# Optimization experiments

Measured on AMD Instinct MI355X. Metric: run time of the kernel, lower is better.

## Reference

```python
import jax, jax.numpy as jnp
import numpy as np

B, S, D = 1, 2048, 2048
H = 16
HD = D // H           # 128
FFN_H = 5632          # int(2*4*D/3) rounded up to multiple of 256
EPS = 1e-5
ROPE_THETA = 10000.0


def rms_norm(x, w, eps=EPS):
    # x * rsqrt(mean(x^2, -1) + eps) * w
    return x * jax.lax.rsqrt(jnp.mean(x * x, axis=-1, keepdims=True) + eps) * w


def apply_rope(x, cos, sin):
    # x: [B, S, H, HD]; cos/sin: [S, HD//2]
    b, s, h, hd = x.shape
    xr = x.reshape(b, s, h, hd // 2, 2)
    x_re, x_im = xr[..., 0], xr[..., 1]
    c = cos[None, :, None, :]
    sn = sin[None, :, None, :]
    o_re = x_re * c - x_im * sn
    o_im = x_re * sn + x_im * c
    return jnp.stack([o_re, o_im], axis=-1).reshape(b, s, h, hd)


def setup_inputs() -> dict:
    key = jax.random.key(0)
    ks = jax.random.split(key, 10)
    x = jax.random.normal(ks[0], (B, S, D), dtype=jnp.float32)
    # RoPE frequencies (Llama-style)
    inv_freq = 1.0 / (ROPE_THETA ** (np.arange(0, HD, 2, dtype=np.float32) / HD))
    angles = np.outer(np.arange(S, dtype=np.float32), inv_freq)  # [S, HD//2]
    freqs_cos = jnp.asarray(np.cos(angles), dtype=jnp.float32)
    freqs_sin = jnp.asarray(np.sin(angles), dtype=jnp.float32)
    # causal mask: 1 = keep, 0 = masked
    mask = jnp.tril(jnp.ones((S, S), dtype=jnp.int32))[None, None]
    sc = 0.02
    return {
        "x": x,
        "freqs_cos": freqs_cos,
        "freqs_sin": freqs_sin,
        "mask": mask,
        "wq": jax.random.normal(ks[1], (D, D), jnp.float32) * sc,
        "wk": jax.random.normal(ks[2], (D, D), jnp.float32) * sc,
        "wv": jax.random.normal(ks[3], (D, D), jnp.float32) * sc,
        "wo": jax.random.normal(ks[4], (D, D), jnp.float32) * sc,
        "w1": jax.random.normal(ks[5], (D, FFN_H), jnp.float32) * sc,
        "w2": jax.random.normal(ks[6], (FFN_H, D), jnp.float32) * sc,
        "w3": jax.random.normal(ks[7], (D, FFN_H), jnp.float32) * sc,
        "attn_norm_w": jnp.ones((D,), jnp.float32),
        "ffn_norm_w": jnp.ones((D,), jnp.float32),
    }


def reference(x, freqs_cos, freqs_sin, mask, wq, wk, wv, wo, w1, w2, w3,
              attn_norm_w, ffn_norm_w):
    b, s, d = x.shape
    # --- attention block ---
    xn = rms_norm(x, attn_norm_w)
    q = (xn @ wq).reshape(b, s, H, HD)
    k = (xn @ wk).reshape(b, s, H, HD)
    v = (xn @ wv).reshape(b, s, H, HD)
    q = apply_rope(q, freqs_cos, freqs_sin)
    k = apply_rope(k, freqs_cos, freqs_sin)
    scores = jnp.einsum('bqhd,bkhd->bhqk', q, k) / jnp.sqrt(jnp.float32(HD))
    scores = jnp.where(mask == 0, -jnp.inf, scores)
    probs = jax.nn.softmax(scores, axis=-1)
    attn = jnp.einsum('bhqk,bkhd->bqhd', probs, v).reshape(b, s, d)
    h = x + attn @ wo
    # --- SwiGLU FFN block ---
    hn = rms_norm(h, ffn_norm_w)
    ff = (jax.nn.silu(hn @ w1) * (hn @ w3)) @ w2
    return h + ff
```

## Files before the change

### kernel.cpp

```cpp
#include <hip/hip_runtime.h>
#include <hip/hip_bf16.h>

typedef __bf16 bf16x8 __attribute__((ext_vector_type(8)));
typedef float f32x4 __attribute__((ext_vector_type(4)));
typedef unsigned short u16x8 __attribute__((ext_vector_type(8)));
typedef unsigned short u16x4 __attribute__((ext_vector_type(4)));

#define DEV static __device__ __forceinline__

DEV unsigned short f2bf(float f) {
    unsigned u = __builtin_bit_cast(unsigned, f);
    u += 0x7fffu + ((u >> 16) & 1u);
    return (unsigned short)(u >> 16);
}
DEV float bf2f(unsigned short h) {
    unsigned u = ((unsigned)h) << 16;
    return __builtin_bit_cast(float, u);
}

DEV void gl2lds16(const void* g, void* l) {
    __builtin_amdgcn_global_load_lds(
        (const __attribute__((address_space(1))) void*)g,
        (__attribute__((address_space(3))) void*)l, 16, 0, 0);
}

#define WAITV(N) asm volatile("s_waitcnt vmcnt(" #N ")" ::: "memory")
#define SBAR()   asm volatile("s_barrier" ::: "memory")

#define STAGE256(KT, SLOT, BUF)                                               \
    {                                                                         \
        const unsigned short* sbase = ((SLOT) & 1)                            \
            ? BT + (size_t)(bn + ((SLOT) >> 1) * 128) * K                     \
            : A  + (size_t)(bm + ((SLOT) >> 1) * 128) * K;                    \
        _Pragma("unroll")                                                     \
        for (int j = 0; j < 2; ++j) {                                         \
            const unsigned short* g = sbase + (size_t)(srow + j * 64) * K     \
                                      + (KT) * 64 + lc;                       \
            gl2lds16(g, &lds[BUF][SLOT][wave * 512 + j * 4096]);              \
        }                                                                     \
    }

#define COMPUTE256(BUF, MH, NH)                                               \
    {                                                                         \
        const char* Ab = (const char*)&lds[BUF][(MH) * 2][0];                 \
        const char* Bb = (const char*)&lds[BUF][(NH) * 2 + 1][0];             \
        bf16x8 a_[4][2], b_[2][2];                                            \
        _Pragma("unroll")                                                     \
        for (int m4 = 0; m4 < 4; ++m4) {                                      \
            _Pragma("unroll")                                                 \
            for (int kk = 0; kk < 2; ++kk)                                    \
                a_[m4][kk] = *(const bf16x8*)(Ab +                            \
                    (wm * 64 + m4 * 16 + lr) * 128 +                          \
                    ((kk * 64 + lg * 16) ^ xsw));                             \
        }                                                                     \
        _Pragma("unroll")                                                     \
        for (int n2 = 0; n2 < 2; ++n2) {                                      \
            _Pragma("unroll")                                                 \
            for (int kk = 0; kk < 2; ++kk)                                    \
                b_[n2][kk] = *(const bf16x8*)(Bb +                            \
                    (wn * 32 + n2 * 16 + lr) * 128 +                          \
                    ((kk * 64 + lg * 16) ^ xsw));                             \
        }                                                                     \
        __builtin_amdgcn_s_setprio(1);                                        \
        _Pragma("unroll")                                                     \
        for (int m4 = 0; m4 < 4; ++m4)                                        \
            _Pragma("unroll")                                                 \
            for (int n2 = 0; n2 < 2; ++n2)                                    \
                _Pragma("unroll")                                             \
                for (int kk = 0; kk < 2; ++kk)                                \
                    acc[(MH) * 4 + m4][(NH) * 2 + n2] =                       \
                        __builtin_amdgcn_mfma_f32_16x16x32_bf16(              \
                            a_[m4][kk], b_[n2][kk],                           \
                            acc[(MH) * 4 + m4][(NH) * 2 + n2], 0, 0, 0);      \
        __builtin_amdgcn_s_setprio(0);                                        \
    }

__global__ __launch_bounds__(512, 2)
void gemm256_bt(const unsigned short* __restrict__ A,
                const unsigned short* __restrict__ BT,
                unsigned short* __restrict__ outB,
                int M, int N, int K)
{
    __shared__ alignas(16) unsigned short lds[2][4][8192];
    const int tid  = threadIdx.x;
    const int lane = tid & 63;
    const int wave = tid >> 6;
    const int wm = wave >> 2;
    const int wn = wave & 3;
    const int lr = lane & 15;
    const int lg = lane >> 4;
    const int lin = blockIdx.y * gridDim.x + blockIdx.x;
    const int cpx = (gridDim.x * gridDim.y) >> 3;
    const int swz = (lin & 7) * cpx + (lin >> 3);
    const int bm = (swz & 7) * 256;
    const int bn = (swz >> 3) * 256;
    const int xsw  = (lr & 7) << 4;
    const int srow = tid >> 3;
    const int lc   = ((tid & 7) ^ (srow & 7)) * 8;

    f32x4 acc[8][4] = {};
    const int NT = K >> 6;

    STAGE256(0, 0, 0); STAGE256(0, 1, 0); STAGE256(0, 2, 0); STAGE256(0, 3, 0);
    for (int kt = 0; kt < NT - 1; ++kt) {
        const int buf = kt & 1, nbuf = buf ^ 1;
        STAGE256(kt + 1, 0, nbuf);
        WAITV(6); SBAR();
        COMPUTE256(buf, 0, 0);
        STAGE256(kt + 1, 1, nbuf);
        WAITV(6); SBAR();
        COMPUTE256(buf, 1, 0);
        STAGE256(kt + 1, 2, nbuf);
        WAITV(6); SBAR();
        COMPUTE256(buf, 1, 1);
        STAGE256(kt + 1, 3, nbuf);
        COMPUTE256(buf, 0, 1);
        SBAR();
    }
    {
        const int buf = (NT - 1) & 1;
        WAITV(4); SBAR();
        COMPUTE256(buf, 0, 0);
        WAITV(2); SBAR();
        COMPUTE256(buf, 1, 0);
        WAITV(0); SBAR();
        COMPUTE256(buf, 1, 1);
        COMPUTE256(buf, 0, 1);
    }

#pragma unroll
    for (int m = 0; m < 8; ++m) {
        const int row = bm + (m >> 2) * 128 + wm * 64 + (m & 3) * 16 + lg * 4;
#pragma unroll
        for (int n = 0; n < 4; ++n) {
            const int col = bn + (n >> 1) * 128 + wn * 32 + (n & 1) * 16 + lr;
#pragma unroll
            for (int r = 0; r < 4; ++r)
                outB[(size_t)(row + r) * N + col] = f2bf(acc[m][n][r]);
        }
    }
}

#define STAGE128D(KT, BUF)                                                    \
    _Pragma("unroll")                                                         \
    for (int sl = 0; sl < 3; ++sl) {                                          \
        const unsigned short* sbase = (sl == 0)                               \
            ? A  + (size_t)bm * K                                             \
            : BT + (size_t)(bn + (sl - 1) * 128) * K;                         \
        _Pragma("unroll")                                                     \
        for (int j = 0; j < 2; ++j) {                                         \
            const unsigned short* g = sbase + (size_t)(srow + j * 64) * K     \
                                      + koff + (KT) * 64 + lc;                \
            gl2lds16(g, &lds[BUF][sl][wave * 512 + j * 4096]);                \
        }                                                                     \
    }

#define COMPUTE128D(BUF)                                                      \
    {                                                                         \
        const char* Ab = (const char*)&lds[BUF][0][0];                        \
        const char* Bb = (const char*)&lds[BUF][1 + (wn >> 1)][0];            \
        bf16x8 a_[4][2], b_[4][2];                                            \
        _Pragma("unroll")                                                     \
        for (int m4 = 0; m4 < 4; ++m4)                                        \
            _Pragma("unroll")                                                 \
            for (int kk = 0; kk < 2; ++kk)                                    \
                a_[m4][kk] = *(const bf16x8*)(Ab +                            \
                    (wm * 64 + m4 * 16 + lr) * 128 +                          \
                    ((kk * 64 + lg * 16) ^ xsw));                             \
        _Pragma("unroll")                                                     \
        for (int n2 = 0; n2 < 4; ++n2)                                        \
            _Pragma("unroll")                                                 \
            for (int kk = 0; kk < 2; ++kk)                                    \
                b_[n2][kk] = *(const bf16x8*)(Bb +                            \
                    ((wn & 1) * 64 + n2 * 16 + lr) * 128 +                    \
                    ((kk * 64 + lg * 16) ^ xsw));                             \
        __builtin_amdgcn_s_setprio(1);                                        \
        _Pragma("unroll")                                                     \
        for (int m4 = 0; m4 < 4; ++m4)                                        \
            _Pragma("unroll")                                                 \
            for (int n2 = 0; n2 < 4; ++n2)                                    \
                _Pragma("unroll")                                             \
                for (int kk = 0; kk < 2; ++kk)                                \
                    acc[m4][n2] = __builtin_amdgcn_mfma_f32_16x16x32_bf16(    \
                        a_[m4][kk], b_[n2][kk], acc[m4][n2], 0, 0, 0);        \
        __builtin_amdgcn_s_setprio(0);                                        \
    }

template <int EPI>
__global__ __launch_bounds__(512, 2)
void gemm128d(const unsigned short* __restrict__ A,
              const unsigned short* __restrict__ BT,
              unsigned short* __restrict__ outB,
              float* __restrict__ outP,
              int M, int N, int K)
{
    __shared__ alignas(16) unsigned short lds[3][3][8192];
    const int tid  = threadIdx.x;
    const int lane = tid & 63;
    const int wave = tid >> 6;
    const int wm = wave >> 2;
    const int wn = wave & 3;
    const int lr = lane & 15;
    const int lg = lane >> 4;
    const int gy  = gridDim.y;
    const int lin = blockIdx.y * gridDim.x + blockIdx.x;
    const int cpx = (gridDim.x * gy) >> 3;
    const int swz = (lin & 7) * cpx + (lin >> 3);
    const int bm = (swz % gy) * 128;
    const int bn = (swz / gy) * 256;
    const int xsw  = (lr & 7) << 4;
    const int srow = tid >> 3;
    const int lc   = ((tid & 7) ^ (srow & 7)) * 8;
    int koff, NT;
    if constexpr (EPI == 1) { const int Kh = K >> 1; koff = blockIdx.z * Kh; NT = Kh >> 6; }
    else                    { koff = 0;              NT = K >> 6; }

    f32x4 acc[4][4] = {};

    STAGE128D(0, 0);
    STAGE128D(1, 1);
    int bc = 0;
    for (int kt = 0; kt + 2 < NT; ++kt) {
        const int nb = (bc == 0) ? 2 : bc - 1;
        STAGE128D(kt + 2, nb);
        WAITV(12); SBAR();
        COMPUTE128D(bc);
        SBAR();
        bc = (bc == 2) ? 0 : bc + 1;
    }
    WAITV(6); SBAR();
    COMPUTE128D(bc);
    SBAR();
    bc = (bc == 2) ? 0 : bc + 1;
    WAITV(0); SBAR();
    COMPUTE128D(bc);

#pragma unroll
    for (int m4 = 0; m4 < 4; ++m4) {
        const int row = bm + wm * 64 + m4 * 16 + lg * 4;
#pragma unroll
        for (int n2 = 0; n2 < 4; ++n2) {
            const int col = bn + wn * 64 + n2 * 16 + lr;
#pragma unroll
            for (int r = 0; r < 4; ++r) {
                if constexpr (EPI == 0) {
                    outB[(size_t)(row + r) * N + col] = f2bf(acc[m4][n2][r]);
                } else if constexpr (EPI == 1) {
                    outP[(size_t)blockIdx.z * M * N + (size_t)(row + r) * N + col] = acc[m4][n2][r];
                } else {
                    const float v  = acc[m4][n2][r];
                    const float vo = __shfl_xor(v, 1);
                    const float x1 = (lr & 1) ? vo : v;
                    const float x3 = (lr & 1) ? v : vo;
                    const float g  = x1 / (1.0f + __expf(-x1)) * x3;
                    if (!(lr & 1))
                        outB[(size_t)(row + r) * (N >> 1) + (col >> 1)] = f2bf(g);
                }
            }
        }
    }
}

__global__ __launch_bounds__(256)
void reduce2_add(const float* res, const float* p, float* out, int n4)
{
    const float4* r4 = (const float4*)res;
    const float4* a4 = (const float4*)p;
    const float4* b4 = (const float4*)(p + (size_t)2048 * 2048);
    float4* o4 = (float4*)out;
    for (int i = blockIdx.x * 256 + threadIdx.x; i < n4; i += gridDim.x * 256) {
        const float4 r = r4[i], a = a4[i], b = b4[i];
        o4[i] = make_float4(r.x + a.x + b.x, r.y + a.y + b.y,
                            r.z + a.z + b.z, r.w + a.w + b.w);
    }
}

__global__ __launch_bounds__(256)
void reduce2_norm(const float* __restrict__ res, const float* __restrict__ p,
                  const float* __restrict__ w, float* __restrict__ hout,
                  unsigned short* __restrict__ nout)
{
    const int row = blockIdx.x, tid = threadIdx.x;
    const float4* r4 = (const float4*)(res + (size_t)row * 2048);
    const float4* a4 = (const float4*)(p   + (size_t)row * 2048);
    const float4* b4 = (const float4*)(p + (size_t)2048 * 2048 + (size_t)row * 2048);
    float4* h4 = (float4*)(hout + (size_t)row * 2048);
    float4 h[2];
    float ss = 0.f;
#pragma unroll
    for (int i = 0; i < 2; ++i) {
        const int idx = i * 256 + tid;
        const float4 r = r4[idx], a = a4[idx], b = b4[idx];
        float4 v = make_float4(r.x + a.x + b.x, r.y + a.y + b.y,
                               r.z + a.z + b.z, r.w + a.w + b.w);
        h[i] = v; h4[idx] = v;
        ss += v.x * v.x + v.y * v.y + v.z * v.z + v.w * v.w;
    }
#pragma unroll
    for (int off = 32; off; off >>= 1) ss += __shfl_xor(ss, off);
    __shared__ float red[4];
    if ((tid & 63) == 0) red[tid >> 6] = ss;
    __syncthreads();
    const float tot = red[0] + red[1] + red[2] + red[3];
    const float sc = rsqrtf(tot * (1.0f / 2048.0f) + 1e-5f);
#pragma unroll
    for (int i = 0; i < 2; ++i) {
        const int idx = i * 256 + tid;
        const float4 wv = ((const float4*)w)[idx];
        u16x4 o;
        o[0] = f2bf(h[i].x * sc * wv.x); o[1] = f2bf(h[i].y * sc * wv.y);
        o[2] = f2bf(h[i].z * sc * wv.z); o[3] = f2bf(h[i].w * sc * wv.w);
        *(u16x4*)(nout + (size_t)row * 2048 + idx * 4) = o;
    }
}

__global__ __launch_bounds__(256)
void rmsnorm_kernel(const float* __restrict__ x, const float* __restrict__ w,
                    unsigned short* __restrict__ out)
{
    const int row = blockIdx.x;
    const int tid = threadIdx.x;
    const float* xr = x + (size_t)row * 2048;
    const float4 a = *reinterpret_cast<const float4*>(xr + tid * 8);
    const float4 b = *reinterpret_cast<const float4*>(xr + tid * 8 + 4);
    float ss = a.x * a.x + a.y * a.y + a.z * a.z + a.w * a.w
             + b.x * b.x + b.y * b.y + b.z * b.z + b.w * b.w;
#pragma unroll
    for (int off = 32; off; off >>= 1) ss += __shfl_xor(ss, off);
    __shared__ float red[4];
    if ((tid & 63) == 0) red[tid >> 6] = ss;
    __syncthreads();
    const float tot = red[0] + red[1] + red[2] + red[3];
    const float sc = rsqrtf(tot * (1.0f / 2048.0f) + 1e-5f);
    const float4 wa = *reinterpret_cast<const float4*>(w + tid * 8);
    const float4 wb = *reinterpret_cast<const float4*>(w + tid * 8 + 4);
    u16x8 o;
    o[0] = f2bf(a.x * sc * wa.x); o[1] = f2bf(a.y * sc * wa.y);
    o[2] = f2bf(a.z * sc * wa.z); o[3] = f2bf(a.w * sc * wa.w);
    o[4] = f2bf(b.x * sc * wb.x); o[5] = f2bf(b.y * sc * wb.y);
    o[6] = f2bf(b.z * sc * wb.z); o[7] = f2bf(b.w * sc * wb.w);
    *reinterpret_cast<u16x8*>(out + (size_t)row * 2048 + tid * 8) = o;
}

__global__ __launch_bounds__(256)
void rope_kernel(unsigned short* __restrict__ t, const float* __restrict__ cs,
                 const float* __restrict__ sn)
{
    const int idx = blockIdx.x * 256 + threadIdx.x;
    const int s   = idx >> 9;
    const int col = (idx & 511) * 8;
    const int i0  = (col & 127) >> 1;
    u16x8 v = *reinterpret_cast<const u16x8*>(t + (size_t)s * 6144 + col);
    const float4 c  = *reinterpret_cast<const float4*>(cs + s * 64 + i0);
    const float4 sv = *reinterpret_cast<const float4*>(sn + s * 64 + i0);
    const float cc[4] = {c.x, c.y, c.z, c.w};
    const float ns[4] = {sv.x, sv.y, sv.z, sv.w};
#pragma unroll
    for (int p = 0; p < 4; ++p) {
        const float re = bf2f(v[2 * p]), im = bf2f(v[2 * p + 1]);
        v[2 * p]     = f2bf(re * cc[p] - im * ns[p]);
        v[2 * p + 1] = f2bf(re * ns[p] + im * cc[p]);
    }
    *reinterpret_cast<u16x8*>(t + (size_t)s * 6144 + col) = v;
}

__global__ __launch_bounds__(256)
void transpose_bf16(const unsigned short* __restrict__ in,
                    unsigned short* __restrict__ out, int M, int N, int ldin)
{
    __shared__ unsigned short t[64][66];
    const int bm = blockIdx.y * 64, bn = blockIdx.x * 64;
    const int tid = threadIdx.x;
    const int r = tid >> 3, c8 = (tid & 7) * 8;
#pragma unroll
    for (int i = 0; i < 2; ++i) {
        const int row = r + i * 32;
        u16x8 v = *reinterpret_cast<const u16x8*>(in + (size_t)(bm + row) * ldin + bn + c8);
#pragma unroll
        for (int e = 0; e < 8; ++e) t[row][c8 + e] = v[e];
    }
    __syncthreads();
#pragma unroll
    for (int i = 0; i < 2; ++i) {
        const int orow = r + i * 32;
        u16x8 v;
#pragma unroll
        for (int e = 0; e < 8; ++e) v[e] = t[c8 + e][orow];
        *reinterpret_cast<u16x8*>(out + (size_t)(bn + orow) * M + bm + c8) = v;
    }
}

__global__ __launch_bounds__(256)
void convT_kernel(const float* __restrict__ w, unsigned short* __restrict__ wT,
                  int K, int N, int rmul, int radd)
{
    __shared__ unsigned short t[64][66];
    const int bk = blockIdx.y * 64, bn = blockIdx.x * 64;
    const int tid = threadIdx.x;
    const int r = tid >> 4, c4 = (tid & 15) * 4;
#pragma unroll
    for (int i = 0; i < 4; ++i) {
        const int row = r + i * 16;
        const float4 v = *reinterpret_cast<const float4*>(w + (size_t)(bk + row) * N + bn + c4);
        t[row][c4 + 0] = f2bf(v.x); t[row][c4 + 1] = f2bf(v.y);
        t[row][c4 + 2] = f2bf(v.z); t[row][c4 + 3] = f2bf(v.w);
    }
    __syncthreads();
#pragma unroll
    for (int i = 0; i < 4; ++i) {
        const int n = r + i * 16;
        u16x4 o;
#pragma unroll
        for (int e = 0; e < 4; ++e) o[e] = t[c4 + e][n];
        *reinterpret_cast<u16x4*>(wT + (size_t)(rmul * (bn + n) + radd) * K + bk + c4) = o;
    }
}

__global__ __launch_bounds__(512)
void flash_attn(const unsigned short* __restrict__ q,
                const unsigned short* __restrict__ k,
                const unsigned short* __restrict__ vT,
                unsigned short* __restrict__ attn)
{
    __shared__ alignas(16) unsigned short Ks[2][64][136];
    __shared__ alignas(16) unsigned short Vs[2][128][72];
    __shared__ alignas(16) unsigned short Ps[8][16][72];

    const int hh = blockIdx.y;
    const int pi = blockIdx.x;
    const int tid = threadIdx.x;
    const int lane = tid & 63, wave = tid >> 6;
    const int qt = (wave >> 2) ? (31 - pi) : pi;
    const int lr = lane & 15, lg = lane >> 4;
    const int q0 = qt * 64 + (wave & 3) * 16;
    const int myNT = qt + 1;
    const int NT   = 32 - pi;

    const int kr0 = tid >> 4, kc0 = (tid & 15) * 8;
    const int vr0 = tid >> 3, vc0 = (tid & 7) * 8;

    bf16x8 qf[4];
#pragma unroll
    for (int c = 0; c < 4; ++c)
        qf[c] = *reinterpret_cast<const bf16x8*>(
            q + (size_t)(q0 + lr) * 6144 + hh * 128 + c * 32 + lg * 8);

    f32x4 oacc[8] = {};
    float m_r[4], l_r[4];
#pragma unroll
    for (int r = 0; r < 4; ++r) { m_r[r] = -INFINITY; l_r[r] = 0.0f; }
    const float scale = 0.08838834764831845f;

    u16x8 kreg0, kreg1, vreg0, vreg1;
    auto gload = [&](int kt) {
        const int kv0 = kt * 64;
        kreg0 = *reinterpret_cast<const u16x8*>(k + (size_t)(kv0 + kr0) * 6144 + hh * 128 + kc0);
        kreg1 = *reinterpret_cast<const u16x8*>(k + (size_t)(kv0 + kr0 + 32) * 6144 + hh * 128 + kc0);
        vreg0 = *reinterpret_cast<const u16x8*>(vT + (size_t)(hh * 128 + vr0) * 2048 + kv0 + vc0);
        vreg1 = *reinterpret_cast<const u16x8*>(vT + (size_t)(hh * 128 + vr0 + 64) * 2048 + kv0 + vc0);
    };
    auto lwrite = [&](int buf) {
        *reinterpret_cast<u16x8*>(&Ks[buf][kr0][kc0])      = kreg0;
        *reinterpret_cast<u16x8*>(&Ks[buf][kr0 + 32][kc0]) = kreg1;
        *reinterpret_cast<u16x8*>(&Vs[buf][vr0][vc0])      = vreg0;
        *reinterpret_cast<u16x8*>(&Vs[buf][vr0 + 64][vc0]) = vreg1;
    };

    gload(0); lwrite(0);
    __syncthreads();

    for (int kt = 0; kt < NT; ++kt) {
        const int buf = kt & 1;
        if (kt + 1 < NT) gload(kt + 1);

        if (kt < myNT) {
            const int kv0 = kt * 64;
            const bool masked = (kt == myNT - 1);
            f32x4 s[4] = {};
            __builtin_amdgcn_s_setprio(1);
#pragma unroll
            for (int ct = 0; ct < 4; ++ct)
#pragma unroll
                for (int c = 0; c < 4; ++c) {
                    const bf16x8 kf = *reinterpret_cast<const bf16x8*>(
                        &Ks[buf][ct * 16 + lr][c * 32 + lg * 8]);
                    s[ct] = __builtin_amdgcn_mfma_f32_16x16x32_bf16(qf[c], kf, s[ct], 0, 0, 0);
                }
            __builtin_amdgcn_s_setprio(0);
#pragma unroll
            for (int ct = 0; ct < 4; ++ct)
#pragma unroll
                for (int r = 0; r < 4; ++r) {
                    float v = s[ct][r] * scale;
                    if (masked) {
                        const int kvg = kv0 + ct * 16 + lr;
                        const int qg  = q0 + lg * 4 + r;
                        if (kvg > qg) v = -INFINITY;
                    }
                    s[ct][r] = v;
                }
            float mn[4], alpha[4], rs[4];
#pragma unroll
            for (int r = 0; r < 4; ++r) {
                float v = fmaxf(fmaxf(s[0][r], s[1][r]), fmaxf(s[2][r], s[3][r]));
                v = fmaxf(v, __shfl_xor(v, 1));
                v = fmaxf(v, __shfl_xor(v, 2));
                v = fmaxf(v, __shfl_xor(v, 4));
                v = fmaxf(v, __shfl_xor(v, 8));
                mn[r] = fmaxf(m_r[r], v);
                alpha[r] = __expf(m_r[r] - mn[r]);
                m_r[r] = mn[r];
                rs[r] = 0.0f;
            }
#pragma unroll
            for (int ct = 0; ct < 4; ++ct)
#pragma unroll
                for (int r = 0; r < 4; ++r) {
                    const float p = __expf(s[ct][r] - mn[r]);
                    s[ct][r] = p;
                    rs[r] += p;
                }
#pragma unroll
            for (int r = 0; r < 4; ++r) {
                float t2 = rs[r];
                t2 += __shfl_xor(t2, 1);
                t2 += __shfl_xor(t2, 2);
                t2 += __shfl_xor(t2, 4);
                t2 += __shfl_xor(t2, 8);
                l_r[r] = l_r[r] * alpha[r] + t2;
            }
#pragma unroll
            for (int ot = 0; ot < 8; ++ot)
#pragma unroll
                for (int r = 0; r < 4; ++r) oacc[ot][r] *= alpha[r];

#pragma unroll
            for (int ct = 0; ct < 4; ++ct)
#pragma unroll
                for (int r = 0; r < 4; ++r)
                    Ps[wave][lg * 4 + r][ct * 16 + lr] = f2bf(s[ct][r]);

            __builtin_amdgcn_s_setprio(1);
#pragma unroll
            for (int c2 = 0; c2 < 2; ++c2) {
                const bf16x8 pf = *reinterpret_cast<const bf16x8*>(
                    &Ps[wave][lr][c2 * 32 + lg * 8]);
#pragma unroll
                for (int ot = 0; ot < 8; ++ot) {
                    const bf16x8 vf = *reinterpret_cast<const bf16x8*>(
                        &Vs[buf][ot * 16 + lr][c2 * 32 + lg * 8]);
                    oacc[ot] = __builtin_amdgcn_mfma_f32_16x16x32_bf16(pf, vf, oacc[ot], 0, 0, 0);
                }
            }
            __builtin_amdgcn_s_setprio(0);
        }

        if (kt + 1 < NT) lwrite(buf ^ 1);
        __syncthreads();
    }

#pragma unroll
    for (int ot = 0; ot < 8; ++ot)
#pragma unroll
        for (int r = 0; r < 4; ++r) {
            const float v = oacc[ot][r] / l_r[r];
            attn[(size_t)(q0 + lg * 4 + r) * 2048 + hh * 128 + ot * 16 + lr] = f2bf(v);
        }
}

extern "C" void kernel_launch(void* const* d_in, const int* in_sizes, int n_in,
                              void* d_out, int out_size, void* d_ws, size_t ws_size,
                              hipStream_t stream)
{
    const float* x    = (const float*)d_in[0];
    const float* fcos = (const float*)d_in[1];
    const float* fsin = (const float*)d_in[2];
    const float* wq  = (const float*)d_in[4];
    const float* wk  = (const float*)d_in[5];
    const float* wv  = (const float*)d_in[6];
    const float* wo  = (const float*)d_in[7];
    const float* w1  = (const float*)d_in[8];
    const float* w2  = (const float*)d_in[9];
    const float* w3  = (const float*)d_in[10];
    const float* anw = (const float*)d_in[11];
    const float* fnw = (const float*)d_in[12];
    float* out = (float*)d_out;

    char* ws = (char*)d_ws;
    size_t off = 0;
    auto alloc = [&](size_t bytes) { void* p = ws + off; off += bytes; return p; };
    const size_t SZ_DD = (size_t)2048 * 2048 * 2;
    const size_t SZ_DF = (size_t)2048 * 5632 * 2;

    unsigned short* wqT  = (unsigned short*)alloc(SZ_DD);
    unsigned short* wkT  = (unsigned short*)alloc(SZ_DD);
    unsigned short* wvT  = (unsigned short*)alloc(SZ_DD);
    unsigned short* woT  = (unsigned short*)alloc(SZ_DD);
    unsigned short* w13T = (unsigned short*)alloc(2 * SZ_DF);
    unsigned short* w2T  = (unsigned short*)alloc(SZ_DF);

    char* reg1 = (char*)alloc((size_t)48 * 1024 * 1024);
    unsigned short* xn   = (unsigned short*)reg1;
    unsigned short* qkv  = (unsigned short*)(reg1 + SZ_DD);
    unsigned short* vTb  = (unsigned short*)(reg1 + SZ_DD + 3 * SZ_DD);
    unsigned short* ab   = (unsigned short*)(reg1 + SZ_DD + 4 * SZ_DD);
    float*          pk   = (float*)reg1;
    unsigned short* hn   = (unsigned short*)(reg1 + 4 * SZ_DD);

    char* reg2 = (char*)alloc(SZ_DF);
    unsigned short* t1 = (unsigned short*)reg2;

    const int N4 = 2048 * 2048 / 4;

    convT_kernel<<<dim3(32, 32), 256, 0, stream>>>(wq, wqT, 2048, 2048, 1, 0);
    convT_kernel<<<dim3(32, 32), 256, 0, stream>>>(wk, wkT, 2048, 2048, 1, 0);
    convT_kernel<<<dim3(32, 32), 256, 0, stream>>>(wv, wvT, 2048, 2048, 1, 0);
    convT_kernel<<<dim3(32, 32), 256, 0, stream>>>(wo, woT, 2048, 2048, 1, 0);
    convT_kernel<<<dim3(88, 32), 256, 0, stream>>>(w1, w13T, 2048, 5632, 2, 0);
    convT_kernel<<<dim3(88, 32), 256, 0, stream>>>(w3, w13T, 2048, 5632, 2, 1);
    convT_kernel<<<dim3(32, 88), 256, 0, stream>>>(w2, w2T, 5632, 2048, 1, 0);

    rmsnorm_kernel<<<2048, 256, 0, stream>>>(x, anw, xn);
    gemm256_bt<<<dim3(24, 8), 512, 0, stream>>>(xn, wqT, qkv, 2048, 6144, 2048);
    rope_kernel<<<4096, 256, 0, stream>>>(qkv, fcos, fsin);
    transpose_bf16<<<dim3(32, 32), 256, 0, stream>>>(qkv + 4096, vTb, 2048, 2048, 6144);
    flash_attn<<<dim3(16, 16), 512, 0, stream>>>(qkv, qkv + 2048, vTb, ab);
    gemm128d<1><<<dim3(8, 16, 2), 512, 0, stream>>>(ab, woT, nullptr, pk, 2048, 2048, 2048);
    reduce2_norm<<<2048, 256, 0, stream>>>(x, pk, fnw, out, hn);

    gemm128d<2><<<dim3(44, 16), 512, 0, stream>>>(hn, w13T, t1, nullptr, 2048, 11264, 2048);
    gemm128d<1><<<dim3(8, 16, 2), 512, 0, stream>>>(t1, w2T, nullptr, pk, 2048, 2048, 5632);
    reduce2_add<<<2048, 256, 0, stream>>>(out, pk, out, N4);
}
```

Before: 439.3 us.

## Software-pipeline LDS reads in gemm128d and use it for QKV projection

```diff
diff --git a/kernel.cpp b/kernel.cpp
--- a/kernel.cpp
+++ b/kernel.cpp
@@ -26,120 +26,6 @@
 
 #define WAITV(N) asm volatile("s_waitcnt vmcnt(" #N ")" ::: "memory")
 #define SBAR()   asm volatile("s_barrier" ::: "memory")
-
-#define STAGE256(KT, SLOT, BUF)                                               \
-    {                                                                         \
-        const unsigned short* sbase = ((SLOT) & 1)                            \
-            ? BT + (size_t)(bn + ((SLOT) >> 1) * 128) * K                     \
-            : A  + (size_t)(bm + ((SLOT) >> 1) * 128) * K;                    \
-        _Pragma("unroll")                                                     \
-        for (int j = 0; j < 2; ++j) {                                         \
-            const unsigned short* g = sbase + (size_t)(srow + j * 64) * K     \
-                                      + (KT) * 64 + lc;                       \
-            gl2lds16(g, &lds[BUF][SLOT][wave * 512 + j * 4096]);              \
-        }                                                                     \
-    }
-
-#define COMPUTE256(BUF, MH, NH)                                               \
-    {                                                                         \
-        const char* Ab = (const char*)&lds[BUF][(MH) * 2][0];                 \
-        const char* Bb = (const char*)&lds[BUF][(NH) * 2 + 1][0];             \
-        bf16x8 a_[4][2], b_[2][2];                                            \
-        _Pragma("unroll")                                                     \
-        for (int m4 = 0; m4 < 4; ++m4) {                                      \
-            _Pragma("unroll")                                                 \
-            for (int kk = 0; kk < 2; ++kk)                                    \
-                a_[m4][kk] = *(const bf16x8*)(Ab +                            \
-                    (wm * 64 + m4 * 16 + lr) * 128 +                          \
-                    ((kk * 64 + lg * 16) ^ xsw));                             \
-        }                                                                     \
-        _Pragma("unroll")                                                     \
-        for (int n2 = 0; n2 < 2; ++n2) {                                      \
-            _Pragma("unroll")                                                 \
-            for (int kk = 0; kk < 2; ++kk)                                    \
-                b_[n2][kk] = *(const bf16x8*)(Bb +                            \
-                    (wn * 32 + n2 * 16 + lr) * 128 +                          \
-                    ((kk * 64 + lg * 16) ^ xsw));                             \
-        }                                                                     \
-        __builtin_amdgcn_s_setprio(1);                                        \
-        _Pragma("unroll")                                                     \
-        for (int m4 = 0; m4 < 4; ++m4)                                        \
-            _Pragma("unroll")                                                 \
-            for (int n2 = 0; n2 < 2; ++n2)                                    \
-                _Pragma("unroll")                                             \
-                for (int kk = 0; kk < 2; ++kk)                                \
-                    acc[(MH) * 4 + m4][(NH) * 2 + n2] =                       \
-                        __builtin_amdgcn_mfma_f32_16x16x32_bf16(              \
-                            a_[m4][kk], b_[n2][kk],                           \
-                            acc[(MH) * 4 + m4][(NH) * 2 + n2], 0, 0, 0);      \
-        __builtin_amdgcn_s_setprio(0);                                        \
-    }
-
-__global__ __launch_bounds__(512, 2)
-void gemm256_bt(const unsigned short* __restrict__ A,
-                const unsigned short* __restrict__ BT,
-                unsigned short* __restrict__ outB,
-                int M, int N, int K)
-{
-    __shared__ alignas(16) unsigned short lds[2][4][8192];
-    const int tid  = threadIdx.x;
-    const int lane = tid & 63;
-    const int wave = tid >> 6;
-    const int wm = wave >> 2;
-    const int wn = wave & 3;
-    const int lr = lane & 15;
-    const int lg = lane >> 4;
-    const int lin = blockIdx.y * gridDim.x + blockIdx.x;
-    const int cpx = (gridDim.x * gridDim.y) >> 3;
-    const int swz = (lin & 7) * cpx + (lin >> 3);
-    const int bm = (swz & 7) * 256;
-    const int bn = (swz >> 3) * 256;
-    const int xsw  = (lr & 7) << 4;
-    const int srow = tid >> 3;
-    const int lc   = ((tid & 7) ^ (srow & 7)) * 8;
-
-    f32x4 acc[8][4] = {};
-    const int NT = K >> 6;
-
-    STAGE256(0, 0, 0); STAGE256(0, 1, 0); STAGE256(0, 2, 0); STAGE256(0, 3, 0);
-    for (int kt = 0; kt < NT - 1; ++kt) {
-        const int buf = kt & 1, nbuf = buf ^ 1;
-        STAGE256(kt + 1, 0, nbuf);
-        WAITV(6); SBAR();
-        COMPUTE256(buf, 0, 0);
-        STAGE256(kt + 1, 1, nbuf);
-        WAITV(6); SBAR();
-        COMPUTE256(buf, 1, 0);
-        STAGE256(kt + 1, 2, nbuf);
-        WAITV(6); SBAR();
-        COMPUTE256(buf, 1, 1);
-        STAGE256(kt + 1, 3, nbuf);
-        COMPUTE256(buf, 0, 1);
-        SBAR();
-    }
-    {
-        const int buf = (NT - 1) & 1;
-        WAITV(4); SBAR();
-        COMPUTE256(buf, 0, 0);
-        WAITV(2); SBAR();
-        COMPUTE256(buf, 1, 0);
-        WAITV(0); SBAR();
-        COMPUTE256(buf, 1, 1);
-        COMPUTE256(buf, 0, 1);
-    }
-
-#pragma unroll
-    for (int m = 0; m < 8; ++m) {
-        const int row = bm + (m >> 2) * 128 + wm * 64 + (m & 3) * 16 + lg * 4;
-#pragma unroll
-        for (int n = 0; n < 4; ++n) {
-            const int col = bn + (n >> 1) * 128 + wn * 32 + (n & 1) * 16 + lr;
-#pragma unroll
-            for (int r = 0; r < 4; ++r)
-                outB[(size_t)(row + r) * N + col] = f2bf(acc[m][n][r]);
-        }
-    }
-}
 
 #define STAGE128D(KT, BUF)                                                    \
     _Pragma("unroll")                                                         \
@@ -155,11 +41,10 @@
         }                                                                     \
     }
 
-#define COMPUTE128D(BUF)                                                      \
+#define DSREAD128(BUF)                                                        \
     {                                                                         \
         const char* Ab = (const char*)&lds[BUF][0][0];                        \
         const char* Bb = (const char*)&lds[BUF][1 + (wn >> 1)][0];            \
-        bf16x8 a_[4][2], b_[4][2];                                            \
         _Pragma("unroll")                                                     \
         for (int m4 = 0; m4 < 4; ++m4)                                        \
             _Pragma("unroll")                                                 \
@@ -174,17 +59,19 @@
                 b_[n2][kk] = *(const bf16x8*)(Bb +                            \
                     ((wn & 1) * 64 + n2 * 16 + lr) * 128 +                    \
                     ((kk * 64 + lg * 16) ^ xsw));                             \
-        __builtin_amdgcn_s_setprio(1);                                        \
+    }
+
+#define MFMA128                                                               \
+    __builtin_amdgcn_s_setprio(1);                                            \
+    _Pragma("unroll")                                                         \
+    for (int m4 = 0; m4 < 4; ++m4)                                            \
         _Pragma("unroll")                                                     \
-        for (int m4 = 0; m4 < 4; ++m4)                                        \
+        for (int n2 = 0; n2 < 4; ++n2)                                        \
             _Pragma("unroll")                                                 \
-            for (int n2 = 0; n2 < 4; ++n2)                                    \
-                _Pragma("unroll")                                             \
-                for (int kk = 0; kk < 2; ++kk)                                \
-                    acc[m4][n2] = __builtin_amdgcn_mfma_f32_16x16x32_bf16(    \
-                        a_[m4][kk], b_[n2][kk], acc[m4][n2], 0, 0, 0);        \
-        __builtin_amdgcn_s_setprio(0);                                        \
-    }
+            for (int kk = 0; kk < 2; ++kk)                                    \
+                acc[m4][n2] = __builtin_amdgcn_mfma_f32_16x16x32_bf16(        \
+                    a_[m4][kk], b_[n2][kk], acc[m4][n2], 0, 0, 0);            \
+    __builtin_amdgcn_s_setprio(0);
 
 template <int EPI>
 __global__ __launch_bounds__(512, 2)
@@ -216,24 +103,30 @@
     else                    { koff = 0;              NT = K >> 6; }
 
     f32x4 acc[4][4] = {};
+    bf16x8 a_[4][2], b_[4][2];
 
     STAGE128D(0, 0);
     STAGE128D(1, 1);
+    WAITV(6); SBAR();
+    DSREAD128(0);
+
     int bc = 0;
-    for (int kt = 0; kt + 2 < NT; ++kt) {
+    for (int kt = 0; kt < NT - 2; ++kt) {
         const int nb = (bc == 0) ? 2 : bc - 1;
         STAGE128D(kt + 2, nb);
-        WAITV(12); SBAR();
-        COMPUTE128D(bc);
-        SBAR();
-        bc = (bc == 2) ? 0 : bc + 1;
-    }
-    WAITV(6); SBAR();
-    COMPUTE128D(bc);
-    SBAR();
-    bc = (bc == 2) ? 0 : bc + 1;
+        MFMA128;
+        WAITV(6); SBAR();
+        const int rb = (bc == 2) ? 0 : bc + 1;
+        DSREAD128(rb);
+        bc = rb;
+    }
+    MFMA128;
     WAITV(0); SBAR();
-    COMPUTE128D(bc);
+    {
+        const int rb = (bc == 2) ? 0 : bc + 1;
+        DSREAD128(rb);
+    }
+    MFMA128;
 
 #pragma unroll
     for (int m4 = 0; m4 < 4; ++m4) {
@@ -621,7 +514,7 @@
     convT_kernel<<<dim3(32, 88), 256, 0, stream>>>(w2, w2T, 5632, 2048, 1, 0);
 
     rmsnorm_kernel<<<2048, 256, 0, stream>>>(x, anw, xn);
-    gemm256_bt<<<dim3(24, 8), 512, 0, stream>>>(xn, wqT, qkv, 2048, 6144, 2048);
+    gemm128d<0><<<dim3(24, 16), 512, 0, stream>>>(xn, wqT, qkv, nullptr, 2048, 6144, 2048);
     rope_kernel<<<4096, 256, 0, stream>>>(qkv, fcos, fsin);
     transpose_bf16<<<dim3(32, 32), 256, 0, stream>>>(qkv + 4096, vTb, 2048, 2048, 6144);
     flash_attn<<<dim3(16, 16), 512, 0, stream>>>(qkv, qkv + 2048, vTb, ab);
```

Measured after the change: 434.7 us. Within noise of the previous version (-1.1%).
